# Optimization experiments

Measured on AMD Instinct MI355X. Metric: run time of the kernel, lower is better.

The kernel has to match this reference:

```python
import jax, jax.numpy as jnp
import numpy as np

M, N, D = 8192, 8192, 256
GAMMA = 1.0 / D  # RBF bandwidth


def setup_inputs() -> dict:
    key = jax.random.key(0)
    k1, k2, k3 = jax.random.split(key, 3)
    Xq = jax.random.normal(k1, (M, D), dtype=jnp.float32)
    Xtrain = jax.random.normal(k2, (N, D), dtype=jnp.float32)
    alpha = jax.random.normal(k3, (N, 1), dtype=jnp.float32)
    return {"Xq": Xq, "Xtrain": Xtrain, "alpha": alpha}


def rbf_kernel(A, B):
    # squared euclidean distances via ||a||^2 + ||b||^2 - 2 a.b  -> [M, N]
    sq_a = jnp.sum(A * A, axis=1, keepdims=True)          # [M,1]
    sq_b = jnp.sum(B * B, axis=1, keepdims=True).T        # [1,N]
    d2 = sq_a + sq_b - 2.0 * jnp.einsum('md,nd->mn', A, B)
    d2 = jnp.maximum(d2, 0.0)
    return jnp.exp(-GAMMA * d2)


def reference(Xq, Xtrain, alpha):
    # forward: kernel(X, self.X) @ self.alpha  -> [M, 1]
    K = rbf_kernel(Xq, Xtrain)
    return K @ alpha
```

## Files before the change

kernel.cpp:

```cpp
#include <hip/hip_runtime.h>
#include <stdint.h>


#define MM 8192
#define NN 8192
#define DD 256
#define GAMMA (1.0f/256.0f)
#define LOG2E 1.44269504088896340736f
#define SCALE_A (2.0f*GAMMA*LOG2E)
#define NEG_G_LOG2E (-GAMMA*LOG2E)

#define NSPLIT 16
#define NPB (NN/NSPLIT)
#define NT_PER (NPB/16)

typedef __bf16 bf16x8 __attribute__((ext_vector_type(8)));
typedef float  f32x4  __attribute__((ext_vector_type(4)));

#define A_OFF  ((size_t)0)
#define B_OFF  ((size_t)4 << 20)
#define W_OFF  ((size_t)8 << 20)
#define EA_OFF (((size_t)8 << 20) + 32768)
#define PART_OFF (((size_t)8 << 20) + 65536)

__device__ __forceinline__ unsigned short f2bf(float f) {
  union { float f; uint32_t u; } x; x.f = f;
  uint32_t u = x.u;
  u += 0x7FFFu + ((u >> 16) & 1u);
  return (unsigned short)(u >> 16);
}
__device__ __forceinline__ uint32_t pack2(float a, float b) {
  return (uint32_t)f2bf(a) | ((uint32_t)f2bf(b) << 16);
}

__global__ __launch_bounds__(256) void prep_kernel(
    const float* __restrict__ Xq, const float* __restrict__ Xt,
    const float* __restrict__ alpha,
    char* __restrict__ Amat, char* __restrict__ Bmat,
    float* __restrict__ w, float* __restrict__ ea)
{
  const int lane = threadIdx.x & 63;
  const int gw = blockIdx.x * 4 + (threadIdx.x >> 6);
  const bool isA = gw < 512;
  const int t = isA ? gw : gw - 512;
  const float* __restrict__ src = isA ? Xq : Xt;
  char* __restrict__ dst = isA ? Amat : Bmat;
  const float sc = isA ? SCALE_A : 1.0f;
  const int n = t * 16 + (lane & 15);
  float ss = 0.f;
#pragma unroll
  for (int r = 0; r < 8; ++r) {
    const int gg = r * 4 + (lane >> 4);
    const float* p = src + (size_t)n * DD + gg * 8;
    const float4 f0 = *(const float4*)p;
    const float4 f1 = *(const float4*)(p + 4);
    ss += f0.x*f0.x + f0.y*f0.y + f0.z*f0.z + f0.w*f0.w
        + f1.x*f1.x + f1.y*f1.y + f1.z*f1.z + f1.w*f1.w;
    uint4 pk;
    pk.x = pack2(f0.x * sc, f0.y * sc); pk.y = pack2(f0.z * sc, f0.w * sc);
    pk.z = pack2(f1.x * sc, f1.y * sc); pk.w = pack2(f1.z * sc, f1.w * sc);
    *(uint4*)(dst + (size_t)t * 8192 + r * 1024 + lane * 16) = pk;
  }
  ss += __shfl_xor(ss, 16, 64);
  ss += __shfl_xor(ss, 32, 64);
  if (lane < 16) {
    if (isA) ea[n] = __builtin_amdgcn_exp2f(NEG_G_LOG2E * ss);
    else     w[n]  = alpha[n] * __builtin_amdgcn_exp2f(NEG_G_LOG2E * ss);
  }
}

__global__ __launch_bounds__(256, 2) void rbf_main(
    const char* __restrict__ Amat, const char* __restrict__ Bmat,
    const float* __restrict__ w, const float* __restrict__ ea,
    float* __restrict__ part)
{
  __shared__ float lds_w[NPB];
  const int tid  = threadIdx.x;
  const int wave = tid >> 6, lane = tid & 63;
  const int quad = lane >> 4, l16 = lane & 15;

  const int b    = blockIdx.x;
  const int xcd  = b & 7, slot = b >> 3;
  const int my   = (xcd & 3) * 8 + (slot & 7);
  const int nx   = (xcd >> 2) * 8 + (slot >> 3);
  const int mt0    = my * 16 + wave * 4;
  const int nt0    = nx * NT_PER;
  const int nbase0 = nx * NPB;

  {
    const float2 wv2 = *(const float2*)(w + nbase0 + tid * 2);
    lds_w[tid * 2]     = wv2.x;
    lds_w[tid * 2 + 1] = wv2.y;
  }

  bf16x8 afrag[4][8];
#pragma unroll
  for (int rt = 0; rt < 4; ++rt)
#pragma unroll
    for (int kc = 0; kc < 8; ++kc) {
      union { uint4 u; bf16x8 v; } cv;
      cv.u = *(const uint4*)(Amat + (size_t)(mt0 + rt) * 8192 + kc * 1024 + lane * 16);
      afrag[rt][kc] = cv.v;
    }

  __syncthreads();

  float outacc[4][4] = {{0,0,0,0},{0,0,0,0},{0,0,0,0},{0,0,0,0}};

  uint4 bufA[8], bufB[8];
  auto loadB = [&](uint4* dst, int ct) {
#pragma unroll
    for (int kc = 0; kc < 8; ++kc)
      dst[kc] = *(const uint4*)(Bmat + (size_t)(nt0 + ct) * 8192 + kc * 1024 + lane * 16);
  };

  const f32x4 fzero = {0.f, 0.f, 0.f, 0.f};
  auto compute = [&](const uint4* buf, int ct) {
    const float wv = lds_w[ct * 16 + l16];
    f32x4 acc[4] = {fzero, fzero, fzero, fzero};
#pragma unroll
    for (int kc = 0; kc < 8; ++kc) {
      union { uint4 u; bf16x8 v; } cv; cv.u = buf[kc];
#pragma unroll
      for (int rt = 0; rt < 4; ++rt)
        acc[rt] = __builtin_amdgcn_mfma_f32_16x16x32_bf16(afrag[rt][kc], cv.v, acc[rt], 0, 0, 0);
    }
#pragma unroll
    for (int rt = 0; rt < 4; ++rt) {
      outacc[rt][0] += wv * __builtin_amdgcn_exp2f(acc[rt][0]);
      outacc[rt][1] += wv * __builtin_amdgcn_exp2f(acc[rt][1]);
      outacc[rt][2] += wv * __builtin_amdgcn_exp2f(acc[rt][2]);
      outacc[rt][3] += wv * __builtin_amdgcn_exp2f(acc[rt][3]);
    }
  };

  loadB(bufA, 0);
  for (int ct = 0; ct < NT_PER; ct += 2) {
    loadB(bufB, ct + 1);
    compute(bufA, ct);
    if (ct + 2 < NT_PER) loadB(bufA, ct + 2);
    compute(bufB, ct + 1);
  }

#pragma unroll
  for (int rt = 0; rt < 4; ++rt)
#pragma unroll
    for (int i = 0; i < 4; ++i) {
      float v = outacc[rt][i];
      v += __shfl_xor(v, 1, 64);
      v += __shfl_xor(v, 2, 64);
      v += __shfl_xor(v, 4, 64);
      v += __shfl_xor(v, 8, 64);
      if (l16 == 0) {
        const int row = my * 256 + wave * 64 + rt * 16 + quad * 4 + i;
        part[(size_t)nx * MM + row] = ea[row] * v;
      }
    }
}

__global__ __launch_bounds__(256) void reduce_kernel(
    const float* __restrict__ part, float* __restrict__ out)
{
  const int row = blockIdx.x * 256 + threadIdx.x;
  float s = 0.f;
#pragma unroll
  for (int i = 0; i < NSPLIT; ++i) s += part[(size_t)i * MM + row];
  out[row] = s;
}

extern "C" void kernel_launch(void* const* d_in, const int* in_sizes, int n_in,
                              void* d_out, int out_size, void* d_ws, size_t ws_size,
                              hipStream_t stream) {
  const float* Xq    = (const float*)d_in[0];
  const float* Xt    = (const float*)d_in[1];
  const float* alpha = (const float*)d_in[2];
  float* out = (float*)d_out;
  char*  ws  = (char*)d_ws;

  char*  Amat = ws + A_OFF;
  char*  Bmat = ws + B_OFF;
  float* w    = (float*)(ws + W_OFF);
  float* ea   = (float*)(ws + EA_OFF);
  float* part = (float*)(ws + PART_OFF);

  hipLaunchKernelGGL(prep_kernel, dim3(256), dim3(256), 0, stream,
                     Xq, Xt, alpha, Amat, Bmat, w, ea);
  hipLaunchKernelGGL(rbf_main, dim3(512), dim3(256), 0, stream,
                     Amat, Bmat, w, ea, part);
  hipLaunchKernelGGL(reduce_kernel, dim3(MM / 256), dim3(256), 0, stream,
                     part, out);
}
```

Measured before the change: 102.8 us.

## Share B tiles across waves via double-buffered LDS staging

Instead of every wave loading the full B tile from global memory into registers, each wave loads a quarter and writes it to a double-buffered LDS region, then all waves read the full tile from LDS. This cuts redundant global/L2 reads of B by four. It adds LDS traffic and a barrier every tile, and reduces register-level prefetch depth.

```diff
diff --git a/kernel.cpp b/kernel.cpp
--- a/kernel.cpp
+++ b/kernel.cpp
@@ -22,6 +22,8 @@
 #define W_OFF  ((size_t)8 << 20)
 #define EA_OFF (((size_t)8 << 20) + 32768)
 #define PART_OFF (((size_t)8 << 20) + 65536)
+
+#define BAR_LGKM() asm volatile("s_waitcnt lgkmcnt(0)\ns_barrier" ::: "memory")
 
 __device__ __forceinline__ unsigned short f2bf(float f) {
   union { float f; uint32_t u; } x; x.f = f;
@@ -74,6 +76,7 @@
     const float* __restrict__ w, const float* __restrict__ ea,
     float* __restrict__ part)
 {
+  __shared__ char  ldsB[2 * 8192];
   __shared__ float lds_w[NPB];
   const int tid  = threadIdx.x;
   const int wave = tid >> 6, lane = tid & 63;
@@ -87,6 +90,20 @@
   const int nt0    = nx * NT_PER;
   const int nbase0 = nx * NPB;
 
+  uint4 greg[2];
+  auto loadG = [&](int ct) {
+    const char* g = Bmat + (size_t)(nt0 + ct) * 8192 + wave * 2048 + lane * 16;
+    greg[0] = *(const uint4*)g;
+    greg[1] = *(const uint4*)(g + 1024);
+  };
+  auto stageW = [&](int buf) {
+    char* l = ldsB + buf * 8192 + wave * 2048 + lane * 16;
+    *(uint4*)l = greg[0];
+    *(uint4*)(l + 1024) = greg[1];
+  };
+
+  loadG(0);
+
   {
     const float2 wv2 = *(const float2*)(w + nbase0 + tid * 2);
     lds_w[tid * 2]     = wv2.x;
@@ -103,24 +120,24 @@
       afrag[rt][kc] = cv.v;
     }
 
-  __syncthreads();
+  stageW(0);
+  loadG(1);
+  BAR_LGKM();
 
   float outacc[4][4] = {{0,0,0,0},{0,0,0,0},{0,0,0,0},{0,0,0,0}};
-
-  uint4 bufA[8], bufB[8];
-  auto loadB = [&](uint4* dst, int ct) {
-#pragma unroll
-    for (int kc = 0; kc < 8; ++kc)
-      dst[kc] = *(const uint4*)(Bmat + (size_t)(nt0 + ct) * 8192 + kc * 1024 + lane * 16);
-  };
-
   const f32x4 fzero = {0.f, 0.f, 0.f, 0.f};
-  auto compute = [&](const uint4* buf, int ct) {
+
+  for (int ct = 0; ct < NT_PER; ++ct) {
+    const int buf = ct & 1;
+    if (ct + 1 < NT_PER) stageW(buf ^ 1);
+    if (ct + 2 < NT_PER) loadG(ct + 2);
+
     const float wv = lds_w[ct * 16 + l16];
     f32x4 acc[4] = {fzero, fzero, fzero, fzero};
 #pragma unroll
     for (int kc = 0; kc < 8; ++kc) {
-      union { uint4 u; bf16x8 v; } cv; cv.u = buf[kc];
+      union { uint4 u; bf16x8 v; } cv;
+      cv.u = *(const uint4*)(ldsB + buf * 8192 + kc * 1024 + lane * 16);
 #pragma unroll
       for (int rt = 0; rt < 4; ++rt)
         acc[rt] = __builtin_amdgcn_mfma_f32_16x16x32_bf16(afrag[rt][kc], cv.v, acc[rt], 0, 0, 0);
@@ -132,14 +149,7 @@
       outacc[rt][2] += wv * __builtin_amdgcn_exp2f(acc[rt][2]);
       outacc[rt][3] += wv * __builtin_amdgcn_exp2f(acc[rt][3]);
     }
-  };
-
-  loadB(bufA, 0);
-  for (int ct = 0; ct < NT_PER; ct += 2) {
-    loadB(bufB, ct + 1);
-    compute(bufA, ct);
-    if (ct + 2 < NT_PER) loadB(bufA, ct + 2);
-    compute(bufB, ct + 1);
+    BAR_LGKM();
   }
 
 #pragma unroll
```

Measured after the change: 117.2 us. 1.14x slower.

## Switch RBF GEMM to 32x32x16 MFMA with chunked triple-buffered B loads

Applied to the files above, without the earlier changes.

Moves the distance GEMM from 16x16x32 to 32x32x16 bf16 MFMA tiles. Each wave now owns 2 row tiles of 32 instead of 4 of 16. The prep kernel's packed fragment layout is rewritten to match the 32-row tiles, and B fragments are streamed in quarter-tile chunks through a 3-slot register ring. The aim is better MFMA throughput per instruction and finer-grained load/compute overlap, at the cost of more accumulator registers and a changed output-row mapping in the epilogue.

```diff
diff --git a/kernel.cpp b/kernel.cpp
--- a/kernel.cpp
+++ b/kernel.cpp
@@ -12,10 +12,11 @@
 
 #define NSPLIT 16
 #define NPB (NN/NSPLIT)
-#define NT_PER (NPB/16)
+#define NT_PER (NPB/32)
+#define NCHUNK (NT_PER*4)
 
 typedef __bf16 bf16x8 __attribute__((ext_vector_type(8)));
-typedef float  f32x4  __attribute__((ext_vector_type(4)));
+typedef float  f32x16 __attribute__((ext_vector_type(16)));
 
 #define A_OFF  ((size_t)0)
 #define B_OFF  ((size_t)4 << 20)
@@ -41,17 +42,17 @@
 {
   const int lane = threadIdx.x & 63;
   const int gw = blockIdx.x * 4 + (threadIdx.x >> 6);
-  const bool isA = gw < 512;
-  const int t = isA ? gw : gw - 512;
+  const bool isA = gw < 256;
+  const int t = isA ? gw : gw - 256;
   const float* __restrict__ src = isA ? Xq : Xt;
   char* __restrict__ dst = isA ? Amat : Bmat;
   const float sc = isA ? SCALE_A : 1.0f;
-  const int n = t * 16 + (lane & 15);
+  const int r = t * 32 + (lane & 31);
+  const int h = lane >> 5;
   float ss = 0.f;
 #pragma unroll
-  for (int r = 0; r < 8; ++r) {
-    const int gg = r * 4 + (lane >> 4);
-    const float* p = src + (size_t)n * DD + gg * 8;
+  for (int s = 0; s < 16; ++s) {
+    const float* p = src + (size_t)r * DD + s * 16 + h * 8;
     const float4 f0 = *(const float4*)p;
     const float4 f1 = *(const float4*)(p + 4);
     ss += f0.x*f0.x + f0.y*f0.y + f0.z*f0.z + f0.w*f0.w
@@ -59,13 +60,12 @@
     uint4 pk;
     pk.x = pack2(f0.x * sc, f0.y * sc); pk.y = pack2(f0.z * sc, f0.w * sc);
     pk.z = pack2(f1.x * sc, f1.y * sc); pk.w = pack2(f1.z * sc, f1.w * sc);
-    *(uint4*)(dst + (size_t)t * 8192 + r * 1024 + lane * 16) = pk;
-  }
-  ss += __shfl_xor(ss, 16, 64);
+    *(uint4*)(dst + (size_t)t * 16384 + s * 1024 + lane * 16) = pk;
+  }
   ss += __shfl_xor(ss, 32, 64);
-  if (lane < 16) {
-    if (isA) ea[n] = __builtin_amdgcn_exp2f(NEG_G_LOG2E * ss);
-    else     w[n]  = alpha[n] * __builtin_amdgcn_exp2f(NEG_G_LOG2E * ss);
+  if (lane < 32) {
+    if (isA) ea[r] = __builtin_amdgcn_exp2f(NEG_G_LOG2E * ss);
+    else     w[r]  = alpha[r] * __builtin_amdgcn_exp2f(NEG_G_LOG2E * ss);
   }
 }
 
@@ -77,13 +77,13 @@
   __shared__ float lds_w[NPB];
   const int tid  = threadIdx.x;
   const int wave = tid >> 6, lane = tid & 63;
-  const int quad = lane >> 4, l16 = lane & 15;
+  const int l32 = lane & 31, h = lane >> 5;
 
   const int b    = blockIdx.x;
   const int xcd  = b & 7, slot = b >> 3;
   const int my   = (xcd & 3) * 8 + (slot & 7);
   const int nx   = (xcd >> 2) * 8 + (slot >> 3);
-  const int mt0    = my * 16 + wave * 4;
+  const int mt0    = my * 8 + wave * 2;
   const int nt0    = nx * NT_PER;
   const int nbase0 = nx * NPB;
 
@@ -93,66 +93,77 @@
     lds_w[tid * 2 + 1] = wv2.y;
   }
 
-  bf16x8 afrag[4][8];
-#pragma unroll
-  for (int rt = 0; rt < 4; ++rt)
-#pragma unroll
-    for (int kc = 0; kc < 8; ++kc) {
+  bf16x8 afrag[2][16];
+#pragma unroll
+  for (int rt = 0; rt < 2; ++rt)
+#pragma unroll
+    for (int s = 0; s < 16; ++s) {
       union { uint4 u; bf16x8 v; } cv;
-      cv.u = *(const uint4*)(Amat + (size_t)(mt0 + rt) * 8192 + kc * 1024 + lane * 16);
-      afrag[rt][kc] = cv.v;
+      cv.u = *(const uint4*)(Amat + (size_t)(mt0 + rt) * 16384 + s * 1024 + lane * 16);
+      afrag[rt][s] = cv.v;
     }
 
   __syncthreads();
 
-  float outacc[4][4] = {{0,0,0,0},{0,0,0,0},{0,0,0,0},{0,0,0,0}};
-
-  uint4 bufA[8], bufB[8];
-  auto loadB = [&](uint4* dst, int ct) {
-#pragma unroll
-    for (int kc = 0; kc < 8; ++kc)
-      dst[kc] = *(const uint4*)(Bmat + (size_t)(nt0 + ct) * 8192 + kc * 1024 + lane * 16);
+  float outacc[2][16];
+#pragma unroll
+  for (int rt = 0; rt < 2; ++rt)
+#pragma unroll
+    for (int i = 0; i < 16; ++i) outacc[rt][i] = 0.f;
+
+  f32x16 acc[2];
+  const f32x16 zero16 = {0,0,0,0,0,0,0,0,0,0,0,0,0,0,0,0};
+  acc[0] = zero16; acc[1] = zero16;
+
+  uint4 ch[3][4];
+  auto loadChunk = [&](int slotIdx, int g) {
+    const int ct = g >> 2, c = g & 3;
+    const char* base = Bmat + (size_t)(nt0 + ct) * 16384 + c * 4096 + (size_t)lane * 16;
+#pragma unroll
+    for (int q = 0; q < 4; ++q)
+      ch[slotIdx][q] = *(const uint4*)(base + q * 1024);
   };
-
-  const f32x4 fzero = {0.f, 0.f, 0.f, 0.f};
-  auto compute = [&](const uint4* buf, int ct) {
-    const float wv = lds_w[ct * 16 + l16];
-    f32x4 acc[4] = {fzero, fzero, fzero, fzero};
-#pragma unroll
-    for (int kc = 0; kc < 8; ++kc) {
-      union { uint4 u; bf16x8 v; } cv; cv.u = buf[kc];
-#pragma unroll
-      for (int rt = 0; rt < 4; ++rt)
-        acc[rt] = __builtin_amdgcn_mfma_f32_16x16x32_bf16(afrag[rt][kc], cv.v, acc[rt], 0, 0, 0);
-    }
-#pragma unroll
-    for (int rt = 0; rt < 4; ++rt) {
-      outacc[rt][0] += wv * __builtin_amdgcn_exp2f(acc[rt][0]);
-      outacc[rt][1] += wv * __builtin_amdgcn_exp2f(acc[rt][1]);
-      outacc[rt][2] += wv * __builtin_amdgcn_exp2f(acc[rt][2]);
-      outacc[rt][3] += wv * __builtin_amdgcn_exp2f(acc[rt][3]);
+  auto mfmaChunk = [&](int slotIdx, int c) {
+#pragma unroll
+    for (int q = 0; q < 4; ++q) {
+      const int s = c * 4 + q;
+      union { uint4 u; bf16x8 v; } cv; cv.u = ch[slotIdx][q];
+#pragma unroll
+      for (int rt = 0; rt < 2; ++rt)
+        acc[rt] = __builtin_amdgcn_mfma_f32_32x32x16_bf16(afrag[rt][s], cv.v, acc[rt], 0, 0, 0);
     }
   };
-
-  loadB(bufA, 0);
-  for (int ct = 0; ct < NT_PER; ct += 2) {
-    loadB(bufB, ct + 1);
-    compute(bufA, ct);
-    if (ct + 2 < NT_PER) loadB(bufA, ct + 2);
-    compute(bufB, ct + 1);
-  }
-
-#pragma unroll
-  for (int rt = 0; rt < 4; ++rt)
-#pragma unroll
-    for (int i = 0; i < 4; ++i) {
+  auto epi = [&](int ct) {
+    const float wv = lds_w[ct * 32 + l32];
+#pragma unroll
+    for (int rt = 0; rt < 2; ++rt) {
+#pragma unroll
+      for (int i = 0; i < 16; ++i)
+        outacc[rt][i] += wv * __builtin_amdgcn_exp2f(acc[rt][i]);
+      acc[rt] = zero16;
+    }
+  };
+
+  loadChunk(0, 0);
+  loadChunk(1, 1);
+  for (int g = 0; g < NCHUNK; ++g) {
+    mfmaChunk(g % 3, g & 3);
+    if (g + 2 < NCHUNK) loadChunk((g + 2) % 3, g + 2);
+    if ((g & 3) == 3) epi(g >> 2);
+  }
+
+#pragma unroll
+  for (int rt = 0; rt < 2; ++rt)
+#pragma unroll
+    for (int i = 0; i < 16; ++i) {
       float v = outacc[rt][i];
       v += __shfl_xor(v, 1, 64);
       v += __shfl_xor(v, 2, 64);
       v += __shfl_xor(v, 4, 64);
       v += __shfl_xor(v, 8, 64);
-      if (l16 == 0) {
-        const int row = my * 256 + wave * 64 + rt * 16 + quad * 4 + i;
+      v += __shfl_xor(v, 16, 64);
+      if (l32 == 0) {
+        const int row = my * 256 + wave * 64 + rt * 32 + (i & 3) + 8 * (i >> 2) + 4 * h;
         part[(size_t)nx * MM + row] = ea[row] * v;
       }
     }
@@ -183,7 +194,7 @@
   float* ea   = (float*)(ws + EA_OFF);
   float* part = (float*)(ws + PART_OFF);
 
-  hipLaunchKernelGGL(prep_kernel, dim3(256), dim3(256), 0, stream,
+  hipLaunchKernelGGL(prep_kernel, dim3(128), dim3(256), 0, stream,
                      Xq, Xt, alpha, Amat, Bmat, w, ea);
   hipLaunchKernelGGL(rbf_main, dim3(512), dim3(256), 0, stream,
                      Amat, Bmat, w, ea, part);
```

Measured after the change: 386.6 us. 3.76x slower.
